# Optimization experiments

Hardware: AMD Instinct MI355X
Metric: run time of the kernel (lower is better)

The kernel has to match this reference:

```python
import jax, jax.numpy as jnp
import numpy as np

B, T, C = 4, 2048, 1024
N_HEAD = 16
HEAD_DIM = C // N_HEAD


def setup_inputs() -> dict:
    key = jax.random.key(0)
    kx, kk, kq, kv, kp = jax.random.split(key, 5)
    s = 1.0 / np.sqrt(C)
    return {
        "x": jax.random.normal(kx, (B, T, C), dtype=jnp.float32),
        "Wk": jax.random.normal(kk, (C, C), dtype=jnp.float32) * s,
        "Wq": jax.random.normal(kq, (C, C), dtype=jnp.float32) * s,
        "Wv": jax.random.normal(kv, (C, C), dtype=jnp.float32) * s,
        "Wp": jax.random.normal(kp, (C, C), dtype=jnp.float32) * s,
    }


def reference(x, Wk, Wq, Wv, Wp):
    b, t, c = x.shape
    # torch nn.Linear(y = x @ W.T); split heads -> [B, H, T, D]
    def heads(w):
        return jnp.einsum("btc,ec->bte", x, w).reshape(b, t, N_HEAD, HEAD_DIM).transpose(0, 2, 1, 3)
    k = heads(Wk)
    q = heads(Wq)
    v = heads(Wv)
    scale = 1.0 / np.sqrt(HEAD_DIM).astype(np.float32)
    att = jnp.einsum("bhqd,bhkd->bhqk", q, k) * scale  # [B,H,T,T]
    causal = jnp.tril(jnp.ones((t, t), dtype=bool))
    att = jnp.where(causal[None, None], att, -jnp.inf)
    att = jax.nn.softmax(att, axis=-1)
    y = jnp.einsum("bhqk,bhkd->bhqd", att, v)  # [B,H,T,D]
    y = y.transpose(0, 2, 1, 3).reshape(b, t, c)
    return jnp.einsum("btc,ec->bte", y, Wp)
```

## Files before the change

kernel.cpp:

```cpp
#include <hip/hip_runtime.h>

typedef __bf16 bf16x8 __attribute__((ext_vector_type(8)));
typedef float f32x4 __attribute__((ext_vector_type(4)));
typedef float f32x16 __attribute__((ext_vector_type(16)));
typedef unsigned short u16x8 __attribute__((ext_vector_type(8)));
typedef unsigned short u16x4 __attribute__((ext_vector_type(4)));
typedef unsigned u32x4 __attribute__((ext_vector_type(4)));

#define BB 4
#define TT 2048
#define CC 1024
#define HH 16
#define DD 64

__device__ __forceinline__ unsigned short f2bf(float f){
  unsigned u = __builtin_bit_cast(unsigned, f);
  u += 0x7FFFu + ((u >> 16) & 1u);
  return (unsigned short)(u >> 16);
}
__device__ __forceinline__ bf16x8 as_bf(u16x8 v){ return __builtin_bit_cast(bf16x8, v); }
__device__ __forceinline__ unsigned cvt_pk(float lo, float hi){
  unsigned r; asm("v_cvt_pk_bf16_f32 %0, %1, %2" : "=v"(r) : "v"(lo), "v"(hi)); return r;
}
__device__ __forceinline__ void pl32swap(unsigned &a, unsigned &b){
  asm("v_permlane32_swap_b32 %0, %1" : "+v"(a), "+v"(b));
}
__device__ __forceinline__ float ex2(float x){
#if __has_builtin(__builtin_amdgcn_exp2f)
  return __builtin_amdgcn_exp2f(x);
#else
  return __expf(x * 0.6931471805599453f);
#endif
}

__global__ __launch_bounds__(256) void cvt_all(const float* __restrict__ x,
                                               const float* __restrict__ Wk,
                                               const float* __restrict__ Wq,
                                               const float* __restrict__ Wv,
                                               const float* __restrict__ Wp,
                                               unsigned short* __restrict__ xb,
                                               unsigned short* __restrict__ wb){
  const int i = blockIdx.x * 256 + threadIdx.x;
  constexpr int EX = (BB*TT*CC)/4;
  const float* src; unsigned short* dst; int off;
  if (i < EX){ src = x; dst = xb; off = i; }
  else {
    const int j = i - EX;
    const int wsel = j >> 18;
    off = j & 262143;
    src = (wsel==0) ? Wk : (wsel==1) ? Wq : (wsel==2) ? Wv : Wp;
    dst = wb + ((size_t)wsel << 20);
  }
  const float4 f = ((const float4*)src)[off];
  u16x4 o; o.x = f2bf(f.x); o.y = f2bf(f.y); o.z = f2bf(f.z); o.w = f2bf(f.w);
  ((u16x4*)dst)[off] = o;
}

template<int NX>
__global__ __launch_bounds__(512, 2) void gemm256q(const unsigned short* __restrict__ A,
                                                   const unsigned short* __restrict__ Bm,
                                                   void* __restrict__ o0, void* __restrict__ o1,
                                                   void* __restrict__ o2){
  constexpr int K = 1024;
  constexpr int NKT = 16;
  constexpr int NWG = NX * 32;
  extern __shared__ unsigned short lds[];
  const int tid = threadIdx.x;
  const int flat = blockIdx.y * NX + blockIdx.x;
  const int swz = (flat & 7) * (NWG / 8) + (flat >> 3);
  const int n0 = (swz % NX) * 256;
  const int m0 = (swz / NX) * 256;
  const int w = tid >> 6, lane = tid & 63, l15 = lane & 15, g = lane >> 4;
  const int wm = (w >> 2) * 128;
  const int wn = (w & 3) * 64;
  const int tsel = n0 >> 10;

  const int sc_q = lane >> 2;
  const int sc_g = (lane & 3) ^ ((lane >> 3) & 3);
  const int rd_cc = g ^ ((l15 >> 1) & 3);

  auto stage = [&](int s, int kt, int ks){
    #pragma unroll
    for (int j = 0; j < 2; ++j){
      const int wl = j*8 + w;
      const int r = wl*16 + sc_q;
      __builtin_amdgcn_global_load_lds(
        (const __attribute__((address_space(1))) void*)(A + (size_t)(m0 + r)*K + kt*64 + ks*32 + sc_g*8),
        (__attribute__((address_space(3))) void*)(lds + s*32768 + ks*8192 + wl*512 + lane*8), 16, 0, 0);
      __builtin_amdgcn_global_load_lds(
        (const __attribute__((address_space(1))) void*)(Bm + (size_t)(n0 + r)*K + kt*64 + ks*32 + sc_g*8),
        (__attribute__((address_space(3))) void*)(lds + s*32768 + 16384 + ks*8192 + wl*512 + lane*8), 16, 0, 0);
    }
  };

  f32x4 acc[8][4] = {};
  stage(0, 0, 0);
  stage(0, 0, 1);

  for (int t = 0; t < NKT; ++t){
    const int s = t & 1;
    #pragma unroll
    for (int ks = 0; ks < 2; ++ks){
      if (t + 1 < NKT){
        stage(s ^ 1, t + 1, ks);
        asm volatile("s_waitcnt vmcnt(8)" ::: "memory");
      } else if (ks == 0){
        asm volatile("s_waitcnt vmcnt(4)" ::: "memory");
      } else {
        asm volatile("s_waitcnt vmcnt(0)" ::: "memory");
      }
      __builtin_amdgcn_s_barrier();
      asm volatile("" ::: "memory");

      const unsigned short* Asl = lds + s*32768 + ks*8192;
      const unsigned short* Bsl = Asl + 16384;
      bf16x8 bfr[4];
      #pragma unroll
      for (int n = 0; n < 4; ++n)
        bfr[n] = as_bf(*(const u16x8*)(Bsl + (wn + n*16 + l15)*32 + rd_cc*8));
      bf16x8 af[8];
      #pragma unroll
      for (int m = 0; m < 8; ++m)
        af[m] = as_bf(*(const u16x8*)(Asl + (wm + m*16 + l15)*32 + rd_cc*8));

      __builtin_amdgcn_s_setprio(1);
      #pragma unroll
      for (int m = 0; m < 8; ++m)
        #pragma unroll
        for (int n = 0; n < 4; ++n)
          acc[m][n] = __builtin_amdgcn_mfma_f32_16x16x32_bf16(af[m], bfr[n], acc[m][n], 0, 0, 0);
      __builtin_amdgcn_s_setprio(0);
    }
  }

  if (tsel == 2){
    const int bq = m0 >> 11;
    const int t0 = m0 & 2047;
    unsigned short* vt = (unsigned short*)o2;
    #pragma unroll
    for (int n = 0; n < 4; ++n){
      const int cg = (n0 & 1023) + wn + n*16 + l15;
      const int h = cg >> 6, d = cg & 63;
      unsigned short* base = vt + ((size_t)(bq*HH + h)*DD + d)*TT;
      #pragma unroll
      for (int m = 0; m < 8; ++m){
        const int t = t0 + wm + m*16 + g*4;
        const int kt = t >> 6;
        const int cch = ((t >> 3) & 7) ^ (d & 7);
        u16x4 pv;
        pv.x = f2bf(acc[m][n][0]); pv.y = f2bf(acc[m][n][1]);
        pv.z = f2bf(acc[m][n][2]); pv.w = f2bf(acc[m][n][3]);
        *(u16x4*)(base + (size_t)kt*64 + cch*8 + (t & 7)) = pv;
      }
    }
    return;
  }

  const float sc = (tsel == 1) ? 0.18033688011112042f : 1.0f;
  unsigned short* outb = (unsigned short*)(tsel == 0 ? o0 : o1);
  #pragma unroll
  for (int m = 0; m < 8; ++m)
    #pragma unroll
    for (int n = 0; n < 4; ++n)
      #pragma unroll
      for (int r = 0; r < 4; ++r){
        const int row = m0 + wm + m*16 + g*4 + r;
        const int col = (n0 & 1023) + wn + n*16 + l15;
        outb[(size_t)row*1024 + col] = f2bf(acc[m][n][r] * sc);
      }
}

template<int NX>
__global__ __launch_bounds__(256) void gemm128(const unsigned short* __restrict__ A,
                                               const unsigned short* __restrict__ Bm,
                                               float* __restrict__ o0){
  constexpr int K = 1024;
  constexpr int NWG = NX * 64;
  __shared__ __align__(16) unsigned short As[128*64];
  __shared__ __align__(16) unsigned short Bs[128*64];
  const int tid = threadIdx.x;
  const int flat = blockIdx.y * NX + blockIdx.x;
  const int swz = (flat & 7) * (NWG / 8) + (flat >> 3);
  const int n0 = (swz % NX) * 128;
  const int m0 = (swz / NX) * 128;
  const int w = tid >> 6, lane = tid & 63, l15 = lane & 15, g = lane >> 4;
  const int wm = (w >> 1) * 64, wn = (w & 1) * 64;

  f32x4 acc[4][4] = {};

  for (int k0 = 0; k0 < K; k0 += 64){
    #pragma unroll
    for (int i = 0; i < 4; ++i){
      const int p = i*256 + tid;
      const int r = p >> 3, c = p & 7;
      const int gc = c ^ (r & 7);
      __builtin_amdgcn_global_load_lds(
        (const __attribute__((address_space(1))) void*)(A + (size_t)(m0 + r)*K + k0 + gc*8),
        (__attribute__((address_space(3))) void*)(As + p*8), 16, 0, 0);
    }
    #pragma unroll
    for (int i = 0; i < 4; ++i){
      const int p = i*256 + tid;
      const int r = p >> 3, c = p & 7;
      const int gc = c ^ (r & 7);
      __builtin_amdgcn_global_load_lds(
        (const __attribute__((address_space(1))) void*)(Bm + (size_t)(n0 + r)*K + k0 + gc*8),
        (__attribute__((address_space(3))) void*)(Bs + p*8), 16, 0, 0);
    }
    __syncthreads();

    bf16x8 af[2][4], bfr[2][4];
    #pragma unroll
    for (int ks = 0; ks < 2; ++ks){
      #pragma unroll
      for (int m = 0; m < 4; ++m){
        const int R = wm + m*16 + l15;
        const int c = (ks*4 + g) ^ (R & 7);
        af[ks][m] = as_bf(*(const u16x8*)(As + R*64 + c*8));
      }
      #pragma unroll
      for (int n = 0; n < 4; ++n){
        const int R = wn + n*16 + l15;
        const int c = (ks*4 + g) ^ (R & 7);
        bfr[ks][n] = as_bf(*(const u16x8*)(Bs + R*64 + c*8));
      }
    }
    #pragma unroll
    for (int ks = 0; ks < 2; ++ks)
      #pragma unroll
      for (int m = 0; m < 4; ++m)
        #pragma unroll
        for (int n = 0; n < 4; ++n)
          acc[m][n] = __builtin_amdgcn_mfma_f32_16x16x32_bf16(af[ks][m], bfr[ks][n], acc[m][n], 0, 0, 0);
    __syncthreads();
  }

  #pragma unroll
  for (int m = 0; m < 4; ++m)
    #pragma unroll
    for (int n = 0; n < 4; ++n)
      #pragma unroll
      for (int r = 0; r < 4; ++r){
        const int row = m0 + wm + m*16 + g*4 + r;
        const int col = n0 + wn + n*16 + l15;
        o0[(size_t)row*1024 + col] = acc[m][n][r];
      }
}

__global__ __launch_bounds__(512, 4) void attn2(const unsigned short* __restrict__ Q,
                                                const unsigned short* __restrict__ Km,
                                                const unsigned short* __restrict__ Vt,
                                                unsigned short* __restrict__ Y){
  __shared__ __align__(16) unsigned short Ks[3][64*64];
  __shared__ __align__(16) unsigned short Vs[3][64*64];
  const int bh = blockIdx.x, b = bh >> 4, h = bh & 15;
  const int yq = blockIdx.y;
  const int qt = (yq < 4) ? (7 - yq) : (yq - 4);
  const int tid = threadIdx.x;
  const int w = tid >> 6, lane = tid & 63, l31 = lane & 31, hi = lane >> 5;
  const int q0 = qt * 256;
  const int wq0 = q0 + w * 32;
  const int wqmax = wq0 + 31;
  const int nkt = 4 * qt + 4;
  const int qg = wq0 + l31;

  const unsigned short* Ksrc = Km + (size_t)b*TT*CC + h*DD;
  const unsigned short* Vsrc = Vt + (size_t)bh*DD*TT;

  auto stage = [&](int buf, int kt){
    const int r = tid >> 3, c = tid & 7;
    const int gc = c ^ (r & 7);
    __builtin_amdgcn_global_load_lds(
      (const __attribute__((address_space(1))) void*)(Ksrc + (size_t)(kt*64 + r)*CC + gc*8),
      (__attribute__((address_space(3))) void*)(&Ks[buf][tid*8]), 16, 0, 0);
    __builtin_amdgcn_global_load_lds(
      (const __attribute__((address_space(1))) void*)(Vsrc + (size_t)r*TT + (size_t)kt*64 + c*8),
      (__attribute__((address_space(3))) void*)(&Vs[buf][tid*8]), 16, 0, 0);
  };

  stage(0, 0);

  const unsigned short* qrow = Q + ((size_t)b*TT + wq0 + l31)*CC + h*DD;
  bf16x8 qf[4];
  #pragma unroll
  for (int ds = 0; ds < 4; ++ds)
    qf[ds] = as_bf(*(const u16x8*)(qrow + 16*ds + 8*hi));

  int koff[4];
  #pragma unroll
  for (int ds = 0; ds < 4; ++ds)
    koff[ds] = l31*64 + (((2*ds + hi) ^ (l31 & 7)) * 8);

  float m_ = -1e30f, l_ = 0.f;
  f32x16 y0 = {}, y1 = {};

  int cb = 0;
  for (int t = 0; t < nkt; ++t){
    const int nx = (cb == 2) ? 0 : cb + 1;
    if (t + 1 < nkt){
      stage(nx, t + 1);
      asm volatile("s_waitcnt vmcnt(2)" ::: "memory");
    } else {
      asm volatile("s_waitcnt vmcnt(0)" ::: "memory");
    }
    __builtin_amdgcn_s_barrier();

    if (t*64 <= wqmax){
      const unsigned short* Kp = &Ks[cb][0];
      const unsigned short* Vp = &Vs[cb][0];

      f32x16 s0 = {}, s1 = {};
      __builtin_amdgcn_s_setprio(1);
      #pragma unroll
      for (int ds = 0; ds < 4; ++ds){
        bf16x8 kf0 = as_bf(*(const u16x8*)(Kp + koff[ds]));
        s0 = __builtin_amdgcn_mfma_f32_32x32x16_bf16(kf0, qf[ds], s0, 0, 0, 0);
        bf16x8 kf1 = as_bf(*(const u16x8*)(Kp + koff[ds] + 2048));
        s1 = __builtin_amdgcn_mfma_f32_32x32x16_bf16(kf1, qf[ds], s1, 0, 0, 0);
      }
      __builtin_amdgcn_s_setprio(0);

      if (t*64 + 63 > wq0){
        const int kb0 = t*64;
        #pragma unroll
        for (int r = 0; r < 16; ++r){
          const int kr = (r & 3) + 8*(r >> 2) + 4*hi;
          if (kb0 + kr      > qg) s0[r] = -1e30f;
          if (kb0 + 32 + kr > qg) s1[r] = -1e30f;
        }
      }

      float tm[8];
      #pragma unroll
      for (int r = 0; r < 8; ++r) tm[r] = fmaxf(fmaxf(s0[r], s0[r+8]), fmaxf(s1[r], s1[r+8]));
      #pragma unroll
      for (int r = 0; r < 4; ++r) tm[r] = fmaxf(tm[r], tm[r+4]);
      float pmax = fmaxf(fmaxf(tm[0], tm[2]), fmaxf(tm[1], tm[3]));
      pmax = fmaxf(pmax, __shfl_xor(pmax, 32));

      if (!__all(pmax <= m_ + 8.f)){
        const float mnew = fmaxf(m_, pmax);
        const float alpha = ex2(m_ - mnew);
        l_ *= alpha;
        #pragma unroll
        for (int r = 0; r < 16; ++r){
          const float ar = __shfl(alpha, (r & 3) + 8*(r >> 2) + 4*hi);
          y0[r] *= ar; y1[r] *= ar;
        }
        m_ = mnew;
      }

      #pragma unroll
      for (int r = 0; r < 16; ++r) s0[r] = ex2(s0[r] - m_);
      #pragma unroll
      for (int r = 0; r < 16; ++r) s1[r] = ex2(s1[r] - m_);
      float ts[8];
      #pragma unroll
      for (int r = 0; r < 8; ++r) ts[r] = (s0[r] + s0[r+8]) + (s1[r] + s1[r+8]);
      #pragma unroll
      for (int r = 0; r < 4; ++r) ts[r] += ts[r+4];
      float rs = (ts[0] + ts[2]) + (ts[1] + ts[3]);
      rs += __shfl_xor(rs, 32);
      l_ += rs;

      __builtin_amdgcn_s_setprio(1);
      #pragma unroll
      for (int m = 0; m < 4; ++m){
        const f32x16 c = (m < 2) ? s0 : s1;
        const int bx = (m & 1) * 8;
        unsigned A0 = cvt_pk(c[bx+0], c[bx+1]);
        unsigned B0 = cvt_pk(c[bx+4], c[bx+5]);
        pl32swap(A0, B0);
        unsigned A1 = cvt_pk(c[bx+2], c[bx+3]);
        unsigned B1 = cvt_pk(c[bx+6], c[bx+7]);
        pl32swap(A1, B1);
        u32x4 pw; pw.x = A0; pw.y = A1; pw.z = B0; pw.w = B1;
        const bf16x8 pa = __builtin_bit_cast(bf16x8, pw);
        bf16x8 vf0 = as_bf(*(const u16x8*)(Vp + koff[m]));
        y0 = __builtin_amdgcn_mfma_f32_32x32x16_bf16(pa, vf0, y0, 0, 0, 0);
        bf16x8 vf1 = as_bf(*(const u16x8*)(Vp + koff[m] + 2048));
        y1 = __builtin_amdgcn_mfma_f32_32x32x16_bf16(pa, vf1, y1, 0, 0, 0);
      }
      __builtin_amdgcn_s_setprio(0);
    }
    cb = nx;
  }

  const float linv = 1.f / l_;
  #pragma unroll
  for (int r = 0; r < 16; ++r){
    const int qlr = (r & 3) + 8*(r >> 2) + 4*hi;
    const float lr = __shfl(linv, qlr);
    unsigned short* yp = Y + ((size_t)b*TT + wq0 + qlr)*CC + h*DD + l31;
    yp[0]  = f2bf(y0[r] * lr);
    yp[32] = f2bf(y1[r] * lr);
  }
}

extern "C" void kernel_launch(void* const* d_in, const int* in_sizes, int n_in,
                              void* d_out, int out_size, void* d_ws, size_t ws_size,
                              hipStream_t stream){
  const float* x  = (const float*)d_in[0];
  const float* Wk = (const float*)d_in[1];
  const float* Wq = (const float*)d_in[2];
  const float* Wv = (const float*)d_in[3];
  const float* Wp = (const float*)d_in[4];

  const size_t E  = (size_t)BB*TT*CC;
  const size_t Wn = (size_t)CC*CC;
  unsigned short* ws  = (unsigned short*)d_ws;
  unsigned short* xb  = ws;
  unsigned short* wkb = xb  + E;
  unsigned short* wqb = wkb + Wn;
  unsigned short* wvb = wqb + Wn;
  unsigned short* wpb = wvb + Wn;
  unsigned short* qb  = wpb + Wn;
  unsigned short* kb  = qb  + E;
  unsigned short* vt  = kb  + E;

  (void)wqb; (void)wvb;

  hipFuncSetAttribute(reinterpret_cast<const void*>(gemm256q<12>),
                      hipFuncAttributeMaxDynamicSharedMemorySize, 131072);

  cvt_all<<<12288, 256, 0, stream>>>(x, Wk, Wq, Wv, Wp, xb, wkb);

  gemm256q<12><<<dim3(12, 32), 512, 131072, stream>>>(xb, wkb, kb, qb, vt);

  unsigned short* yb = xb;
  attn2<<<dim3(BB*HH, TT/256), 512, 0, stream>>>(qb, kb, vt, yb);

  gemm128<8><<<dim3(8, 64), 256, 0, stream>>>(yb, wpb, (float*)d_out);
}
```

Measured before the change: 153.7 us.

## Use four-stage LDS ring with register double-buffered fragments in GEMM

```diff
diff --git a/kernel.cpp b/kernel.cpp
--- a/kernel.cpp
+++ b/kernel.cpp
@@ -62,7 +62,6 @@
                                                    void* __restrict__ o0, void* __restrict__ o1,
                                                    void* __restrict__ o2){
   constexpr int K = 1024;
-  constexpr int NKT = 16;
   constexpr int NWG = NX * 32;
   extern __shared__ unsigned short lds[];
   const int tid = threadIdx.x;
@@ -86,52 +85,69 @@
       const int r = wl*16 + sc_q;
       __builtin_amdgcn_global_load_lds(
         (const __attribute__((address_space(1))) void*)(A + (size_t)(m0 + r)*K + kt*64 + ks*32 + sc_g*8),
-        (__attribute__((address_space(3))) void*)(lds + s*32768 + ks*8192 + wl*512 + lane*8), 16, 0, 0);
+        (__attribute__((address_space(3))) void*)(lds + s*16384 + wl*512 + lane*8), 16, 0, 0);
       __builtin_amdgcn_global_load_lds(
         (const __attribute__((address_space(1))) void*)(Bm + (size_t)(n0 + r)*K + kt*64 + ks*32 + sc_g*8),
-        (__attribute__((address_space(3))) void*)(lds + s*32768 + 16384 + ks*8192 + wl*512 + lane*8), 16, 0, 0);
+        (__attribute__((address_space(3))) void*)(lds + s*16384 + 8192 + wl*512 + lane*8), 16, 0, 0);
     }
   };
 
+  int aoff[8], boff[4];
+  #pragma unroll
+  for (int m = 0; m < 8; ++m) aoff[m] = (wm + m*16 + l15)*32 + rd_cc*8;
+  #pragma unroll
+  for (int n = 0; n < 4; ++n) boff[n] = 8192 + (wn + n*16 + l15)*32 + rd_cc*8;
+
+  auto dsread = [&](int sbase, bf16x8* af, bf16x8* bfr){
+    const unsigned short* base = lds + sbase;
+    #pragma unroll
+    for (int n = 0; n < 4; ++n) bfr[n] = as_bf(*(const u16x8*)(base + boff[n]));
+    #pragma unroll
+    for (int m = 0; m < 8; ++m) af[m] = as_bf(*(const u16x8*)(base + aoff[m]));
+  };
+
   f32x4 acc[8][4] = {};
-  stage(0, 0, 0);
-  stage(0, 0, 1);
-
-  for (int t = 0; t < NKT; ++t){
-    const int s = t & 1;
-    #pragma unroll
-    for (int ks = 0; ks < 2; ++ks){
-      if (t + 1 < NKT){
-        stage(s ^ 1, t + 1, ks);
-        asm volatile("s_waitcnt vmcnt(8)" ::: "memory");
-      } else if (ks == 0){
-        asm volatile("s_waitcnt vmcnt(4)" ::: "memory");
-      } else {
-        asm volatile("s_waitcnt vmcnt(0)" ::: "memory");
-      }
-      __builtin_amdgcn_s_barrier();
-      asm volatile("" ::: "memory");
-
-      const unsigned short* Asl = lds + s*32768 + ks*8192;
-      const unsigned short* Bsl = Asl + 16384;
-      bf16x8 bfr[4];
+  auto mfma32 = [&](bf16x8* af, bf16x8* bfr){
+    __builtin_amdgcn_s_setprio(1);
+    #pragma unroll
+    for (int m = 0; m < 8; ++m)
       #pragma unroll
       for (int n = 0; n < 4; ++n)
-        bfr[n] = as_bf(*(const u16x8*)(Bsl + (wn + n*16 + l15)*32 + rd_cc*8));
-      bf16x8 af[8];
-      #pragma unroll
-      for (int m = 0; m < 8; ++m)
-        af[m] = as_bf(*(const u16x8*)(Asl + (wm + m*16 + l15)*32 + rd_cc*8));
-
-      __builtin_amdgcn_s_setprio(1);
-      #pragma unroll
-      for (int m = 0; m < 8; ++m)
-        #pragma unroll
-        for (int n = 0; n < 4; ++n)
-          acc[m][n] = __builtin_amdgcn_mfma_f32_16x16x32_bf16(af[m], bfr[n], acc[m][n], 0, 0, 0);
-      __builtin_amdgcn_s_setprio(0);
-    }
-  }
+        acc[m][n] = __builtin_amdgcn_mfma_f32_16x16x32_bf16(af[m], bfr[n], acc[m][n], 0, 0, 0);
+    __builtin_amdgcn_s_setprio(0);
+  };
+
+  bf16x8 afA[8], bfA[4], afB[8], bfB[4];
+
+  stage(0, 0, 0); stage(1, 0, 1); stage(2, 1, 0);
+  asm volatile("s_waitcnt vmcnt(8)" ::: "memory");
+  __builtin_amdgcn_s_barrier();
+  dsread(0, afA, bfA);
+
+#define PHASE(SSTG, KT, KS, VMC, SRD, AF_U, BF_U, AF_R, BF_R)      \
+  do {                                                             \
+    if (SSTG >= 0) stage(SSTG, KT, KS);                            \
+    asm volatile("s_waitcnt vmcnt(" #VMC ")" ::: "memory");        \
+    asm volatile("s_waitcnt lgkmcnt(0)" ::: "memory");             \
+    __builtin_amdgcn_s_barrier();                                  \
+    __builtin_amdgcn_sched_barrier(0);                             \
+    mfma32(AF_U, BF_U);                                            \
+    dsread((SRD)*16384, AF_R, BF_R);                               \
+  } while (0)
+
+  for (int t = 0; t < 14; t += 2){
+    PHASE(3, t+1, 1, 8, 1, afA, bfA, afB, bfB);
+    PHASE(0, t+2, 0, 8, 2, afB, bfB, afA, bfA);
+    PHASE(1, t+2, 1, 8, 3, afA, bfA, afB, bfB);
+    PHASE(2, t+3, 0, 8, 0, afB, bfB, afA, bfA);
+  }
+  PHASE( 3, 15, 1, 8, 1, afA, bfA, afB, bfB);
+  PHASE(-1,  0, 0, 4, 2, afB, bfB, afA, bfA);
+  PHASE(-1,  0, 0, 0, 3, afA, bfA, afB, bfB);
+  asm volatile("s_waitcnt lgkmcnt(0)" ::: "memory");
+  __builtin_amdgcn_sched_barrier(0);
+  mfma32(afB, bfB);
+#undef PHASE
 
   if (tsel == 2){
     const int bq = m0 >> 11;
```

Result: no change. 152.6 us (median of 2 runs) (-0.7%).

## Restructure QKV GEMM into 128x256 tiles with six-stage LDS pipeline

Applied to the files above, without the earlier changes.

```diff
diff --git a/kernel.cpp b/kernel.cpp
--- a/kernel.cpp
+++ b/kernel.cpp
@@ -56,22 +56,20 @@
   ((u16x4*)dst)[off] = o;
 }
 
-template<int NX>
-__global__ __launch_bounds__(512, 2) void gemm256q(const unsigned short* __restrict__ A,
-                                                   const unsigned short* __restrict__ Bm,
-                                                   void* __restrict__ o0, void* __restrict__ o1,
-                                                   void* __restrict__ o2){
+__global__ __launch_bounds__(512, 2) void gemmqkv(const unsigned short* __restrict__ A,
+                                                  const unsigned short* __restrict__ Bm,
+                                                  void* __restrict__ o0, void* __restrict__ o1,
+                                                  void* __restrict__ o2){
   constexpr int K = 1024;
-  constexpr int NKT = 16;
-  constexpr int NWG = NX * 32;
+  constexpr int NX = 12, NWG = 768;
   extern __shared__ unsigned short lds[];
   const int tid = threadIdx.x;
   const int flat = blockIdx.y * NX + blockIdx.x;
   const int swz = (flat & 7) * (NWG / 8) + (flat >> 3);
   const int n0 = (swz % NX) * 256;
-  const int m0 = (swz / NX) * 256;
+  const int m0 = (swz / NX) * 128;
   const int w = tid >> 6, lane = tid & 63, l15 = lane & 15, g = lane >> 4;
-  const int wm = (w >> 2) * 128;
+  const int wm = (w >> 2) * 64;
   const int wn = (w & 3) * 64;
   const int tsel = n0 >> 10;
 
@@ -79,59 +77,74 @@
   const int sc_g = (lane & 3) ^ ((lane >> 3) & 3);
   const int rd_cc = g ^ ((l15 >> 1) & 3);
 
-  auto stage = [&](int s, int kt, int ks){
+  auto stage = [&](int s, int h){
+    const int kk = h * 32;
+    {
+      const int r = w*16 + sc_q;
+      __builtin_amdgcn_global_load_lds(
+        (const __attribute__((address_space(1))) void*)(A + (size_t)(m0 + r)*K + kk + sc_g*8),
+        (__attribute__((address_space(3))) void*)(lds + s*12288 + w*512 + lane*8), 16, 0, 0);
+    }
     #pragma unroll
     for (int j = 0; j < 2; ++j){
       const int wl = j*8 + w;
       const int r = wl*16 + sc_q;
       __builtin_amdgcn_global_load_lds(
-        (const __attribute__((address_space(1))) void*)(A + (size_t)(m0 + r)*K + kt*64 + ks*32 + sc_g*8),
-        (__attribute__((address_space(3))) void*)(lds + s*32768 + ks*8192 + wl*512 + lane*8), 16, 0, 0);
-      __builtin_amdgcn_global_load_lds(
-        (const __attribute__((address_space(1))) void*)(Bm + (size_t)(n0 + r)*K + kt*64 + ks*32 + sc_g*8),
-        (__attribute__((address_space(3))) void*)(lds + s*32768 + 16384 + ks*8192 + wl*512 + lane*8), 16, 0, 0);
+        (const __attribute__((address_space(1))) void*)(Bm + (size_t)(n0 + r)*K + kk + sc_g*8),
+        (__attribute__((address_space(3))) void*)(lds + s*12288 + 4096 + wl*512 + lane*8), 16, 0, 0);
     }
   };
 
-  f32x4 acc[8][4] = {};
-  stage(0, 0, 0);
-  stage(0, 0, 1);
-
-  for (int t = 0; t < NKT; ++t){
-    const int s = t & 1;
-    #pragma unroll
-    for (int ks = 0; ks < 2; ++ks){
-      if (t + 1 < NKT){
-        stage(s ^ 1, t + 1, ks);
-        asm volatile("s_waitcnt vmcnt(8)" ::: "memory");
-      } else if (ks == 0){
-        asm volatile("s_waitcnt vmcnt(4)" ::: "memory");
-      } else {
-        asm volatile("s_waitcnt vmcnt(0)" ::: "memory");
-      }
-      __builtin_amdgcn_s_barrier();
-      asm volatile("" ::: "memory");
-
-      const unsigned short* Asl = lds + s*32768 + ks*8192;
-      const unsigned short* Bsl = Asl + 16384;
-      bf16x8 bfr[4];
+  int aoff[4], boff[4];
+  #pragma unroll
+  for (int m = 0; m < 4; ++m) aoff[m] = (wm + m*16 + l15)*32 + rd_cc*8;
+  #pragma unroll
+  for (int n = 0; n < 4; ++n) boff[n] = 4096 + (wn + n*16 + l15)*32 + rd_cc*8;
+
+  auto dsread = [&](int s, bf16x8* af, bf16x8* bfr){
+    const unsigned short* base = lds + s*12288;
+    #pragma unroll
+    for (int n = 0; n < 4; ++n) bfr[n] = as_bf(*(const u16x8*)(base + boff[n]));
+    #pragma unroll
+    for (int m = 0; m < 4; ++m) af[m] = as_bf(*(const u16x8*)(base + aoff[m]));
+  };
+
+  f32x4 acc[4][4] = {};
+  auto mfma16 = [&](bf16x8* af, bf16x8* bfr){
+    __builtin_amdgcn_s_setprio(1);
+    #pragma unroll
+    for (int m = 0; m < 4; ++m)
       #pragma unroll
       for (int n = 0; n < 4; ++n)
-        bfr[n] = as_bf(*(const u16x8*)(Bsl + (wn + n*16 + l15)*32 + rd_cc*8));
-      bf16x8 af[8];
-      #pragma unroll
-      for (int m = 0; m < 8; ++m)
-        af[m] = as_bf(*(const u16x8*)(Asl + (wm + m*16 + l15)*32 + rd_cc*8));
-
-      __builtin_amdgcn_s_setprio(1);
-      #pragma unroll
-      for (int m = 0; m < 8; ++m)
-        #pragma unroll
-        for (int n = 0; n < 4; ++n)
-          acc[m][n] = __builtin_amdgcn_mfma_f32_16x16x32_bf16(af[m], bfr[n], acc[m][n], 0, 0, 0);
-      __builtin_amdgcn_s_setprio(0);
-    }
-  }
+        acc[m][n] = __builtin_amdgcn_mfma_f32_16x16x32_bf16(af[m], bfr[n], acc[m][n], 0, 0, 0);
+    __builtin_amdgcn_s_setprio(0);
+  };
+
+  bf16x8 afA[4], bfA[4], afB[4], bfB[4];
+
+  stage(0,0); stage(1,1); stage(2,2); stage(3,3); stage(4,4);
+  asm volatile("s_waitcnt vmcnt(12)" ::: "memory");
+  __builtin_amdgcn_s_barrier();
+  dsread(0, afA, bfA);
+
+#define PH(P, VMC)                                                  \
+  do {                                                              \
+    asm volatile("s_waitcnt lgkmcnt(0)" ::: "memory");              \
+    asm volatile("s_waitcnt vmcnt(" #VMC ")" ::: "memory");         \
+    __builtin_amdgcn_s_barrier();                                   \
+    __builtin_amdgcn_sched_barrier(0);                              \
+    if ((P) + 5 <= 31) stage(((P) + 5) % 6, (P) + 5);               \
+    mfma16(((P) & 1) ? afB : afA, ((P) & 1) ? bfB : bfA);           \
+    if ((P) + 1 <= 31) dsread(((P) + 1) % 6,                        \
+                              ((P) & 1) ? afA : afB,                \
+                              ((P) & 1) ? bfA : bfB);               \
+  } while (0)
+
+  PH(0,9);  PH(1,9);  PH(2,9);  PH(3,9);  PH(4,9);  PH(5,9);  PH(6,9);  PH(7,9);
+  PH(8,9);  PH(9,9);  PH(10,9); PH(11,9); PH(12,9); PH(13,9); PH(14,9); PH(15,9);
+  PH(16,9); PH(17,9); PH(18,9); PH(19,9); PH(20,9); PH(21,9); PH(22,9); PH(23,9);
+  PH(24,9); PH(25,9); PH(26,9); PH(27,9); PH(28,6); PH(29,3); PH(30,0); PH(31,0);
+#undef PH
 
   if (tsel == 2){
     const int bq = m0 >> 11;
@@ -143,7 +156,7 @@
       const int h = cg >> 6, d = cg & 63;
       unsigned short* base = vt + ((size_t)(bq*HH + h)*DD + d)*TT;
       #pragma unroll
-      for (int m = 0; m < 8; ++m){
+      for (int m = 0; m < 4; ++m){
         const int t = t0 + wm + m*16 + g*4;
         const int kt = t >> 6;
         const int cch = ((t >> 3) & 7) ^ (d & 7);
@@ -159,7 +172,7 @@
   const float sc = (tsel == 1) ? 0.18033688011112042f : 1.0f;
   unsigned short* outb = (unsigned short*)(tsel == 0 ? o0 : o1);
   #pragma unroll
-  for (int m = 0; m < 8; ++m)
+  for (int m = 0; m < 4; ++m)
     #pragma unroll
     for (int n = 0; n < 4; ++n)
       #pragma unroll
@@ -420,12 +433,12 @@
 
   (void)wqb; (void)wvb;
 
-  hipFuncSetAttribute(reinterpret_cast<const void*>(gemm256q<12>),
-                      hipFuncAttributeMaxDynamicSharedMemorySize, 131072);
+  hipFuncSetAttribute(reinterpret_cast<const void*>(gemmqkv),
+                      hipFuncAttributeMaxDynamicSharedMemorySize, 147456);
 
   cvt_all<<<12288, 256, 0, stream>>>(x, Wk, Wq, Wv, Wp, xb, wkb);
 
-  gemm256q<12><<<dim3(12, 32), 512, 131072, stream>>>(xb, wkb, kb, qb, vt);
+  gemmqkv<<<dim3(12, 64), 512, 147456, stream>>>(xb, wkb, kb, qb, vt);
 
   unsigned short* yb = xb;
   attn2<<<dim3(BB*HH, TT/256), 512, 0, stream>>>(qb, kb, vt, yb);
```

After: 160.8 us. 4.6% more time.
